# Performance work log

Hardware: AMD Instinct MI355X
Metric: run time of the kernel (lower is better)

Reference implementation:

```python
import jax, jax.numpy as jnp
import numpy as np

B, T = 32, 1000
NN, NB, CTX = 512, 16, 64
EMB = 256
DCAT = 3 * EMB
H, L = 256, 4
PN, PB = 512, 2
S, V = 8, 64


def setup_inputs() -> dict:
    key = jax.random.key(0)
    ks = jax.random.split(key, 20)
    r = lambda i, shape, sc=1.0: jax.random.normal(ks[i], shape, dtype=jnp.float32) * sc
    nu_log = jnp.log(-jnp.log(jax.random.uniform(ks[8], (L, H), minval=0.5, maxval=0.95)))
    inp = {
        'neural_input': r(0, (B, T, NN)),
        'behavior_input': r(1, (B, T, NB)),
        'session_id': jax.random.randint(ks[2], (B,), 0, V),
        'subject_id': jax.random.randint(ks[3], (B,), 0, S),
        'session_table': r(4, (V, CTX), 0.02),
        'neural_W': r(5, (S, EMB, NN), 1.0 / np.sqrt(NN)),
        'neural_b': jnp.zeros((S, EMB), jnp.float32),
        'behavior_W': r(6, (S, EMB, NB), 1.0 / np.sqrt(NB)),
        'behavior_b': jnp.zeros((S, EMB), jnp.float32),
        'ctx_W': r(7, (EMB, CTX), 1.0 / np.sqrt(CTX)),
        'ctx_b': jnp.zeros((EMB,), jnp.float32),
        'nu_log': nu_log,
        'theta_log': jnp.log(jax.random.uniform(ks[9], (L, H), minval=1e-4, maxval=6.283)),
        'gamma_log': 0.5 * jnp.log1p(-jnp.exp(-2.0 * jnp.exp(nu_log))),
        'B_re': r(10, (L, H, DCAT), 1.0 / np.sqrt(2 * DCAT)),
        'B_im': r(11, (L, H, DCAT), 1.0 / np.sqrt(2 * DCAT)),
        'C_re': r(12, (L, DCAT, H), 1.0 / np.sqrt(H)),
        'C_im': r(13, (L, DCAT, H), 1.0 / np.sqrt(H)),
        'D_skip': r(14, (L, DCAT)),
        'dec_n_W': r(15, (S, PN, DCAT), 1.0 / np.sqrt(DCAT)),
        'dec_n_b': jnp.zeros((S, PN), jnp.float32),
        'dec_b_W': r(16, (S, PB, DCAT), 1.0 / np.sqrt(DCAT)),
        'dec_b_b': jnp.zeros((S, PB), jnp.float32),
    }
    return inp


def _lru(u, nu_log, theta_log, gamma_log, B_re, B_im, C_re, C_im, D_skip):
    # Linear Recurrent Unit: complex diagonal recurrence x_t = lam*x_{t-1} + gamma*B u_t
    lam = jnp.exp(-jnp.exp(nu_log) + 1j * jnp.exp(theta_log))  # [H]
    g = jnp.exp(gamma_log)[:, None]
    Bu = (jnp.einsum('bti,hi->bth', u, B_re * g)
          + 1j * jnp.einsum('bti,hi->bth', u, B_im * g))  # [B,T,H] complex

    def step(x, bu_t):
        x = lam * x + bu_t
        return x, x

    x0 = jnp.zeros((u.shape[0], nu_log.shape[0]), jnp.complex64)
    _, xs = jax.lax.scan(step, x0, jnp.swapaxes(Bu, 0, 1))
    xs = jnp.swapaxes(xs, 0, 1)  # [B,T,H]
    y = jnp.einsum('bth,oh->bto', xs, C_re + 1j * C_im).real + D_skip * u
    return y


def _forward(neural_input, behavior_input, session_table, neural_W, neural_b,
             behavior_W, behavior_b, ctx_W, ctx_b, nu_log, theta_log, gamma_log,
             B_re, B_im, C_re, C_im, D_skip, dec_n_W, dec_n_b, dec_b_W, dec_b_b,
             session_id, subject_id):
    act = jax.nn.relu
    Bsz, Ts, _ = neural_input.shape
    # session-token embedding -> context embedder (Linear is per-timestep, so embed once then broadcast)
    ctx = act(session_table[session_id] @ ctx_W.T + ctx_b)  # [B,EMB]
    ctx = jnp.broadcast_to(ctx[:, None, :], (Bsz, Ts, ctx.shape[-1]))
    # subject-routed embedders: gather per-sample weights, one batched GEMM
    en = act(jnp.einsum('btf,bef->bte', neural_input, neural_W[subject_id])
             + neural_b[subject_id][:, None, :])
    eb = act(jnp.einsum('btf,bef->bte', behavior_input, behavior_W[subject_id])
             + behavior_b[subject_id][:, None, :])
    h = jnp.concatenate([en, eb, ctx], axis=-1)  # [B,T,3*EMB]
    for l in range(nu_log.shape[0]):
        h = _lru(h, nu_log[l], theta_log[l], gamma_log[l],
                 B_re[l], B_im[l], C_re[l], C_im[l], D_skip[l])
    # subject-routed decoders
    pred_n = jax.nn.softplus(jnp.einsum('btd,bod->bto', h, dec_n_W[subject_id])
                             + dec_n_b[subject_id][:, None, :])
    pred_b = (jnp.einsum('btd,bod->bto', h, dec_b_W[subject_id])
              + dec_b_b[subject_id][:, None, :])
    return pred_n, pred_b


def reference(neural_input, behavior_input, session_id, subject_id, session_table,
              neural_W, neural_b, behavior_W, behavior_b, ctx_W, ctx_b,
              nu_log, theta_log, gamma_log, B_re, B_im, C_re, C_im, D_skip,
              dec_n_W, dec_n_b, dec_b_W, dec_b_b):
    return _forward(neural_input, behavior_input, session_table, neural_W, neural_b,
                    behavior_W, behavior_b, ctx_W, ctx_b, nu_log, theta_log, gamma_log,
                    B_re, B_im, C_re, C_im, D_skip, dec_n_W, dec_n_b, dec_b_W, dec_b_b,
                    session_id, subject_id)
```

## Files before the change

kernel.cpp:

```cpp
#include <hip/hip_runtime.h>

typedef __bf16 bf16;
typedef __bf16 bf16x8 __attribute__((ext_vector_type(8)));
typedef float f32x4 __attribute__((ext_vector_type(4)));

#define AS1 __attribute__((address_space(1)))
#define AS3 __attribute__((address_space(3)))

__device__ __forceinline__ void gll16(const void* g, void* l) {
    __builtin_amdgcn_global_load_lds((const AS1 void*)g, (AS3 void*)l, 16, 0, 0);
}

template<int EPI>
__device__ __forceinline__
void gemm_body(const bf16* __restrict__ Abase, long long aBstride, int lda,
               const bf16* __restrict__ Wbase, long long wSstride,
               const float* __restrict__ biasBase, int biasStride,
               void* __restrict__ Cbase, long long cBstride, int ldc,
               const float* __restrict__ dskip,
               const bf16* __restrict__ Ubase, long long uBstride,
               const int* __restrict__ subj,
               int M, int K, int nbn, char* smem)
{
    const int tid = threadIdx.x;
    const int lane = tid & 63;
    const int wid = tid >> 6;
    const int wm = wid >> 1, wn = wid & 1;
    const int l15 = lane & 15, lhi = lane >> 4;
    const int sw7 = l15 & 7;

    const int nwg = gridDim.x;
    const int bid = blockIdx.x;
    const int q = nwg >> 3, r = nwg & 7;
    const int xcd = bid & 7;
    const int sw = xcd * q + (xcd < r ? xcd : r) + (bid >> 3);
    const int m0 = (sw / nbn) * 256;
    const int n0 = (sw % nbn) * 128;

    const int b = blockIdx.z;
    const int s = subj ? subj[b] : 0;
    const bf16* A = Abase + (size_t)b * aBstride;
    const bf16* W = Wbase + (size_t)s * wSstride;
    const float* bias = biasBase ? biasBase + (size_t)s * biasStride : nullptr;
    const bf16* U = Ubase ? Ubase + (size_t)b * uBstride : nullptr;
    const size_t coff = (size_t)b * cBstride;
    const int Mc = M - 1;

    f32x4 acc[4][4];
    #pragma unroll
    for (int i = 0; i < 4; ++i)
        #pragma unroll
        for (int j = 0; j < 4; ++j)
            acc[i][j] = f32x4{0.f, 0.f, 0.f, 0.f};

    int rA[4], rB[4];
    #pragma unroll
    for (int f = 0; f < 4; ++f) {
        rA[f] = (wm*64 + f*16 + l15) * 128;
        rB[f] = (wn*64 + f*16 + l15) * 128;
    }

    const int sub  = tid >> 3;
    const int slot = tid & 7;
    const int ldsw = (wid << 10);

    auto stage = [&](int kt, int bufo) {
        #pragma unroll
        for (int c = 0; c < 4; ++c) {
            const int row = c*64 + sub;
            const int gk = (kt << 6) + ((slot ^ (row & 7)) << 3);
            int ar = m0 + row; if (ar > Mc) ar = Mc;
            gll16(A + (size_t)ar * lda + gk, smem + bufo + c*8192 + ldsw);
        }
        #pragma unroll
        for (int c = 0; c < 2; ++c) {
            const int row = c*64 + sub;
            const int gk = (kt << 6) + ((slot ^ (row & 7)) << 3);
            gll16(W + (size_t)(n0 + row) * K + gk, smem + bufo + 32768 + c*8192 + ldsw);
        }
    };

    const int nkt = K >> 6;
    stage(0, 0);
    if (nkt > 1) stage(1, 49152);
    asm volatile("s_waitcnt vmcnt(6)" ::: "memory");
    __builtin_amdgcn_s_barrier();

    int curo = 0, nno = 98304;
    for (int t = 0; t < nkt; ++t) {
        if (t + 2 < nkt) stage(t + 2, nno);

        const char* cb = smem + curo;
        #pragma unroll
        for (int kk = 0; kk < 2; ++kk) {
            const int so_ = (((kk << 2) | lhi) ^ sw7) << 4;
            bf16x8 af[4], bg[4];
            #pragma unroll
            for (int f = 0; f < 4; ++f) af[f] = *(const bf16x8*)(cb + rA[f] + so_);
            #pragma unroll
            for (int g = 0; g < 4; ++g) bg[g] = *(const bf16x8*)(cb + 32768 + rB[g] + so_);
            #pragma unroll
            for (int i = 0; i < 4; ++i)
                #pragma unroll
                for (int j = 0; j < 4; ++j)
                    acc[i][j] = __builtin_amdgcn_mfma_f32_16x16x32_bf16(
                        af[i], bg[j], acc[i][j], 0, 0, 0);
        }

        if (t + 2 < nkt) {
            asm volatile("s_waitcnt vmcnt(6)" ::: "memory");
        } else if (t + 1 < nkt) {
            asm volatile("s_waitcnt vmcnt(0)" ::: "memory");
        }
        if (t + 1 < nkt) __builtin_amdgcn_s_barrier();

        curo = (curo == 98304) ? 0 : curo + 49152;
        nno  = (nno  == 98304) ? 0 : nno  + 49152;
    }

    __syncthreads();
    #pragma unroll
    for (int i = 0; i < 4; ++i) {
        #pragma unroll
        for (int j = 0; j < 4; ++j) {
            const int colb = (wn*64 + j*16 + l15) * 2;
            const f32x4 v = acc[i][j];
            #pragma unroll
            for (int qq = 0; qq < 4; ++qq) {
                const int row = wm*64 + i*16 + lhi*4 + qq;
                const int ad = row*256 + (colb & 15) + ((((colb >> 4) ^ (row & 7)) & 15) << 4);
                *(bf16*)(smem + ad) = (bf16)v[qq];
            }
        }
    }
    __syncthreads();

    #pragma unroll
    for (int u = 0; u < 8; ++u) {
        const int chunk = u*512 + tid;
        const int rr = chunk >> 4, ss = chunk & 15;
        const int gr = m0 + rr;
        if (gr >= M) continue;
        const int col = n0 + ss*8;
        const bf16x8 v = *(const bf16x8*)(smem + rr*256 + ((ss ^ (rr & 7)) << 4));
        if constexpr (EPI == 0) {
            const size_t ci = coff + (size_t)gr * ldc + col;
            *(bf16x8*)((bf16*)Cbase + ci) = v;
        } else if constexpr (EPI == 1) {
            const float4 b0 = *(const float4*)(bias + col);
            const float4 b1 = *(const float4*)(bias + col + 4);
            bf16x8 o;
            o[0] = (bf16)fmaxf((float)v[0] + b0.x, 0.f);
            o[1] = (bf16)fmaxf((float)v[1] + b0.y, 0.f);
            o[2] = (bf16)fmaxf((float)v[2] + b0.z, 0.f);
            o[3] = (bf16)fmaxf((float)v[3] + b0.w, 0.f);
            o[4] = (bf16)fmaxf((float)v[4] + b1.x, 0.f);
            o[5] = (bf16)fmaxf((float)v[5] + b1.y, 0.f);
            o[6] = (bf16)fmaxf((float)v[6] + b1.z, 0.f);
            o[7] = (bf16)fmaxf((float)v[7] + b1.w, 0.f);
            const size_t ci = coff + (size_t)gr * ldc + col;
            *(bf16x8*)((bf16*)Cbase + ci) = o;
        } else if constexpr (EPI == 2) {
            const bf16x8 uv = *(const bf16x8*)(U + (size_t)gr * ldc + col);
            const float4 d0 = *(const float4*)(dskip + col);
            const float4 d1 = *(const float4*)(dskip + col + 4);
            bf16x8 o;
            o[0] = (bf16)((float)v[0] + d0.x * (float)uv[0]);
            o[1] = (bf16)((float)v[1] + d0.y * (float)uv[1]);
            o[2] = (bf16)((float)v[2] + d0.z * (float)uv[2]);
            o[3] = (bf16)((float)v[3] + d0.w * (float)uv[3]);
            o[4] = (bf16)((float)v[4] + d1.x * (float)uv[4]);
            o[5] = (bf16)((float)v[5] + d1.y * (float)uv[5]);
            o[6] = (bf16)((float)v[6] + d1.z * (float)uv[6]);
            o[7] = (bf16)((float)v[7] + d1.w * (float)uv[7]);
            const size_t ci = coff + (size_t)gr * ldc + col;
            *(bf16x8*)((bf16*)Cbase + ci) = o;
        } else {
            const float4 b0 = *(const float4*)(bias + col);
            const float4 b1 = *(const float4*)(bias + col + 4);
            float xv[8];
            xv[0] = (float)v[0] + b0.x; xv[1] = (float)v[1] + b0.y;
            xv[2] = (float)v[2] + b0.z; xv[3] = (float)v[3] + b0.w;
            xv[4] = (float)v[4] + b1.x; xv[5] = (float)v[5] + b1.y;
            xv[6] = (float)v[6] + b1.z; xv[7] = (float)v[7] + b1.w;
            float4 o0, o1;
            #pragma unroll
            for (int e = 0; e < 8; ++e) {
                const float x = xv[e];
                const float sp = fmaxf(x, 0.f) + log1pf(expf(-fabsf(x)));
                if (e < 4) ((float*)&o0)[e] = sp; else ((float*)&o1)[e-4] = sp;
            }
            const size_t ci = coff + (size_t)gr * ldc + col;
            *(float4*)((float*)Cbase + ci) = o0;
            *(float4*)((float*)Cbase + ci + 4) = o1;
        }
    }
}

#define GEMM_WRAP(NAME, EPI)                                                     \
__global__ __launch_bounds__(512, 2)                                             \
void NAME(const bf16* __restrict__ Abase, long long aBstride, int lda,           \
          const bf16* __restrict__ Wbase, long long wSstride,                    \
          const float* __restrict__ biasBase, int biasStride,                    \
          void* __restrict__ Cbase, long long cBstride, int ldc,                 \
          const float* __restrict__ dskip,                                       \
          const bf16* __restrict__ Ubase, long long uBstride,                    \
          const int* __restrict__ subj, int M, int K, int nbn)                   \
{                                                                                \
    __shared__ char smem[147456];                                                \
    gemm_body<EPI>(Abase, aBstride, lda, Wbase, wSstride, biasBase, biasStride,  \
                   Cbase, cBstride, ldc, dskip, Ubase, uBstride, subj,           \
                   M, K, nbn, smem);                                             \
}
GEMM_WRAP(gemm_en,  1)
GEMM_WRAP(gemm_bu,  0)
GEMM_WRAP(gemm_y,   2)
GEMM_WRAP(gemm_dec, 3)

__global__ void scan_finals(const bf16* __restrict__ Bu,
                            const float* __restrict__ nu_log,
                            const float* __restrict__ theta_log,
                            float2* __restrict__ finals)
{
    const int g = blockIdx.x * 256 + threadIdx.x;
    const int h = g & 255;
    const int c = (g >> 8) % 40;
    const int b = g / 10240;
    const float a  = expf(nu_log[h]);
    const float th = expf(theta_log[h]);
    const float mag = expf(-a);
    const float lre = mag * cosf(th), lim = mag * sinf(th);
    float xre = 0.f, xim = 0.f;
    const bf16* p = Bu + ((size_t)(b*1000 + c*25)) * 512 + h;
    for (int i = 0; i < 25; ++i) {
        const float bre = (float)p[0], bim = (float)p[256];
        const float nre = lre*xre - lim*xim + bre;
        const float nim = lre*xim + lim*xre + bim;
        xre = nre; xim = nim;
        p += 512;
    }
    finals[(b*40 + c)*256 + h] = make_float2(xre, xim);
}

__global__ void scan_carry(const float2* __restrict__ finals,
                           float2* __restrict__ carry,
                           const float* __restrict__ nu_log,
                           const float* __restrict__ theta_log)
{
    const int g = blockIdx.x * 256 + threadIdx.x;
    const int h = g & 255;
    const int b = g >> 8;
    const float a  = expf(nu_log[h]);
    const float th = expf(theta_log[h]);
    const float mag = expf(-25.f * a);
    const float ang = 25.f * th;
    const float cre = mag * cosf(ang), cim = mag * sinf(ang);
    float pre = 0.f, pim = 0.f;
    for (int c = 0; c < 40; ++c) {
        const int idx = (b*40 + c)*256 + h;
        carry[idx] = make_float2(pre, pim);
        const float2 f = finals[idx];
        const float nre = f.x + cre*pre - cim*pim;
        const float nim = f.y + cre*pim + cim*pre;
        pre = nre; pim = nim;
    }
}

__global__ void scan_emit(const bf16* __restrict__ Bu,
                          const float2* __restrict__ carry,
                          const float* __restrict__ nu_log,
                          const float* __restrict__ theta_log,
                          bf16* __restrict__ xs)
{
    const int g = blockIdx.x * 256 + threadIdx.x;
    const int h = g & 255;
    const int c = (g >> 8) % 40;
    const int b = g / 10240;
    const float a  = expf(nu_log[h]);
    const float th = expf(theta_log[h]);
    const float mag = expf(-a);
    const float lre = mag * cosf(th), lim = mag * sinf(th);
    const float2 cr = carry[(b*40 + c)*256 + h];
    float xre = cr.x, xim = cr.y;
    const bf16* p = Bu + ((size_t)(b*1000 + c*25)) * 512 + h;
    bf16* qp = xs + ((size_t)(b*1000 + c*25)) * 512 + h;
    for (int i = 0; i < 25; ++i) {
        const float bre = (float)p[0], bim = (float)p[256];
        const float nre = lre*xre - lim*xim + bre;
        const float nim = lre*xim + lim*xre + bim;
        xre = nre; xim = nim;
        qp[0] = (bf16)xre; qp[256] = (bf16)xim;
        p += 512; qp += 512;
    }
}

__global__ void cast8_kern(const float* __restrict__ src, bf16* __restrict__ dst, int n8)
{
    const int i = blockIdx.x * 256 + threadIdx.x;
    if (i >= n8) return;
    const float4* s = (const float4*)src + (size_t)i*2;
    const float4 v0 = s[0], v1 = s[1];
    bf16x8 o;
    o[0] = (bf16)v0.x; o[1] = (bf16)v0.y; o[2] = (bf16)v0.z; o[3] = (bf16)v0.w;
    o[4] = (bf16)v1.x; o[5] = (bf16)v1.y; o[6] = (bf16)v1.z; o[7] = (bf16)v1.w;
    *((bf16x8*)dst + i) = o;
}

__global__ void packWB_kern(const float* __restrict__ Bre, const float* __restrict__ Bim,
                            const float* __restrict__ glog, bf16* __restrict__ WB)
{
    const int idx = blockIdx.x * 256 + threadIdx.x;
    if (idx >= 4*512*768) return;
    const int l = idx / (512*768);
    const int r = idx - l*(512*768);
    const int n = r / 768;
    const int k = r - n*768;
    float v;
    if (n < 256) v = Bre[((size_t)(l*256 + n))*768 + k] * expf(glog[l*256 + n]);
    else         v = Bim[((size_t)(l*256 + (n-256)))*768 + k] * expf(glog[l*256 + (n-256)]);
    WB[idx] = (bf16)v;
}

__global__ void packWC_kern(const float* __restrict__ Cre, const float* __restrict__ Cim,
                            bf16* __restrict__ WC)
{
    const int idx = blockIdx.x * 256 + threadIdx.x;
    if (idx >= 4*768*512) return;
    const int l = idx / (768*512);
    const int r = idx - l*(768*512);
    const int o = r / 512;
    const int k = r - o*512;
    const float v = (k < 256) ? Cre[((size_t)(l*768 + o))*256 + k]
                              : -Cim[((size_t)(l*768 + o))*256 + (k - 256)];
    WC[idx] = (bf16)v;
}

__global__ void ctx_kern(const float* __restrict__ st, const int* __restrict__ sess,
                         const float* __restrict__ cW, const float* __restrict__ cb,
                         float* __restrict__ ctx)
{
    const int b = blockIdx.x;
    const int e = threadIdx.x;
    const int sid = sess[b];
    const float* r = st + (size_t)sid * 64;
    const float* w = cW + (size_t)e * 64;
    float acc = cb[e];
    #pragma unroll 8
    for (int i = 0; i < 64; ++i) acc += r[i] * w[i];
    ctx[b*256 + e] = fmaxf(acc, 0.f);
}

__global__ void ebctx_kern(const float* __restrict__ behav,
                           const float* __restrict__ bW,
                           const float* __restrict__ bB,
                           const int* __restrict__ subj,
                           const float* __restrict__ ctx,
                           bf16* __restrict__ h0)
{
    const int b  = blockIdx.x >> 3;
    const int tc = blockIdx.x & 7;
    const int e = threadIdx.x;
    const int s = subj[b];
    float wreg[16];
    const float* w = bW + ((size_t)(s*256) + e)*16;
    #pragma unroll
    for (int i = 0; i < 16; ++i) wreg[i] = w[i];
    const float bb_ = bB[s*256 + e];
    const bf16 cx = (bf16)ctx[b*256 + e];
    const int t0 = tc * 125;
    for (int t = t0; t < t0 + 125; ++t) {
        const int blk = b*1000 + t;
        const float* bi = behav + (size_t)blk * 16;
        float acc = bb_;
        #pragma unroll
        for (int i = 0; i < 16; ++i) acc += bi[i] * wreg[i];
        bf16* hp = h0 + (size_t)blk * 768;
        hp[256 + e] = (bf16)fmaxf(acc, 0.f);
        hp[512 + e] = cx;
    }
}

__global__ void predb_kern(const bf16* __restrict__ h, const float* __restrict__ W,
                           const float* __restrict__ bb, const int* __restrict__ subj,
                           float* __restrict__ out)
{
    const int lane = threadIdx.x & 63;
    const int wid  = threadIdx.x >> 6;
    const int row  = blockIdx.x * 4 + wid;
    const int b = row / 1000;
    const int s = subj[b];
    const bf16* hr = h + (size_t)row * 768;
    const float* w0 = W + (size_t)(s*2) * 768;
    const float* w1 = w0 + 768;
    float a0 = 0.f, a1 = 0.f;
    #pragma unroll
    for (int j = 0; j < 12; ++j) {
        const int idx = j*64 + lane;
        const float hv = (float)hr[idx];
        a0 += hv * w0[idx];
        a1 += hv * w1[idx];
    }
    #pragma unroll
    for (int m = 32; m >= 1; m >>= 1) {
        a0 += __shfl_xor(a0, m);
        a1 += __shfl_xor(a1, m);
    }
    if (lane == 0) {
        out[(size_t)row*2 + 0] = a0 + bb[s*2 + 0];
        out[(size_t)row*2 + 1] = a1 + bb[s*2 + 1];
    }
}

extern "C" void kernel_launch(void* const* d_in, const int* in_sizes, int n_in,
                              void* d_out, int out_size, void* d_ws, size_t ws_size,
                              hipStream_t stream)
{
    const float* neural_input   = (const float*)d_in[0];
    const float* behavior_input = (const float*)d_in[1];
    const int*   session_id     = (const int*)d_in[2];
    const int*   subject_id     = (const int*)d_in[3];
    const float* session_table  = (const float*)d_in[4];
    const float* neural_W  = (const float*)d_in[5];
    const float* neural_b  = (const float*)d_in[6];
    const float* behavior_W = (const float*)d_in[7];
    const float* behavior_b = (const float*)d_in[8];
    const float* ctx_W = (const float*)d_in[9];
    const float* ctx_b = (const float*)d_in[10];
    const float* nu_log    = (const float*)d_in[11];
    const float* theta_log = (const float*)d_in[12];
    const float* gamma_log = (const float*)d_in[13];
    const float* B_re = (const float*)d_in[14];
    const float* B_im = (const float*)d_in[15];
    const float* C_re = (const float*)d_in[16];
    const float* C_im = (const float*)d_in[17];
    const float* D_skip = (const float*)d_in[18];
    const float* dec_n_W = (const float*)d_in[19];
    const float* dec_n_b = (const float*)d_in[20];
    const float* dec_b_W = (const float*)d_in[21];
    const float* dec_b_b = (const float*)d_in[22];
    float* out = (float*)d_out;

    char* ws = (char*)d_ws;
    size_t off = 0;
    auto alloc = [&](size_t bytes) -> char* {
        char* p = ws + off;
        off += (bytes + 255) & ~(size_t)255;
        return p;
    };
    bf16*   Wn      = (bf16*)alloc((size_t)8*256*512*2);
    bf16*   Wd      = (bf16*)alloc((size_t)8*512*768*2);
    bf16*   WB      = (bf16*)alloc((size_t)4*512*768*2);
    bf16*   WC      = (bf16*)alloc((size_t)4*768*512*2);
    float*  ctxbuf  = (float*)alloc((size_t)32*256*4);
    bf16*   hA      = (bf16*)alloc((size_t)32*1000*768*2);
    bf16*   hB      = (bf16*)alloc((size_t)32*1000*768*2);
    bf16*   xs      = (bf16*)alloc((size_t)32*1000*512*2);
    float2* finals  = (float2*)alloc((size_t)32*40*256*8);
    float2* carry   = (float2*)alloc((size_t)32*40*256*8);
    bf16*   Bu      = (bf16*)alloc((size_t)32*1000*512*2);
    bf16*   nbf     = Bu;

    cast8_kern<<<dim3(512),   256, 0, stream>>>(neural_W, Wn, 131072);
    cast8_kern<<<dim3(1536),  256, 0, stream>>>(dec_n_W,  Wd, 393216);
    packWB_kern<<<dim3(6144), 256, 0, stream>>>(B_re, B_im, gamma_log, WB);
    packWC_kern<<<dim3(6144), 256, 0, stream>>>(C_re, C_im, WC);
    ctx_kern<<<dim3(32), 256, 0, stream>>>(session_table, session_id, ctx_W, ctx_b, ctxbuf);
    cast8_kern<<<dim3(8000), 256, 0, stream>>>(neural_input, nbf, 2048000);

    ebctx_kern<<<dim3(256), 256, 0, stream>>>(behavior_input, behavior_W, behavior_b,
                                              subject_id, ctxbuf, hA);
    gemm_en<<<dim3(8, 1, 32), 512, 0, stream>>>(
        nbf, 512000LL, 512, Wn, 131072LL, neural_b, 256,
        hA, 768000LL, 768, nullptr, nullptr, 0LL, subject_id, 1000, 512, 2);

    for (int l = 0; l < 4; ++l) {
        const bf16* hin  = (l & 1) ? hB : hA;
        bf16*       hout = (l & 1) ? hA : hB;
        gemm_bu<<<dim3(500, 1, 1), 512, 0, stream>>>(
            hin, 0LL, 768, WB + (size_t)l*393216, 0LL, nullptr, 0,
            Bu, 0LL, 512, nullptr, nullptr, 0LL, nullptr, 32000, 768, 4);
        scan_finals<<<dim3(1280), 256, 0, stream>>>(Bu, nu_log + l*256, theta_log + l*256, finals);
        scan_carry<<<dim3(32), 256, 0, stream>>>(finals, carry, nu_log + l*256, theta_log + l*256);
        scan_emit<<<dim3(1280), 256, 0, stream>>>(Bu, carry, nu_log + l*256, theta_log + l*256, xs);
        gemm_y<<<dim3(750, 1, 1), 512, 0, stream>>>(
            xs, 0LL, 512, WC + (size_t)l*393216, 0LL, nullptr, 0,
            hout, 0LL, 768, D_skip + l*768, hin, 0LL, nullptr, 32000, 512, 6);
    }

    gemm_dec<<<dim3(16, 1, 32), 512, 0, stream>>>(
        hA, 768000LL, 768, Wd, 393216LL, dec_n_b, 512,
        out, 512000LL, 512, nullptr, nullptr, 0LL, subject_id, 1000, 768, 4);
    predb_kern<<<dim3(8000), 256, 0, stream>>>(hA, dec_b_W, dec_b_b, subject_id,
                                               out + 16384000);
}
```

Baseline: 610.6 us.

## Fuse three-pass chunked LRU scan into one kernel with in-block carry propagation

Replaces the finals/carry/emit kernel trio with a single kernel in which each block owns 32 hidden channels of one batch row, splits time into 8 chunks of 125 steps, and propagates chunk carries through shared memory. This removes two launches per layer and the global round-trips for the finals and carry buffers. The cost is much less parallelism: 256 blocks instead of 1280, each thread running a serial 125-step chain twice, and 32-channel loads that are less coalesced. It also switches the decoder softplus to fast __logf/__expf intrinsics, trading some accuracy.

After: 616.9 us. About the same (+1.0%).

```diff
diff --git a/kernel.cpp b/kernel.cpp
--- a/kernel.cpp
+++ b/kernel.cpp
@@ -1,6 +1,7 @@
 #include <hip/hip_runtime.h>
 
 typedef __bf16 bf16;
+typedef __bf16 bf16x2 __attribute__((ext_vector_type(2)));
 typedef __bf16 bf16x8 __attribute__((ext_vector_type(8)));
 typedef float f32x4 __attribute__((ext_vector_type(4)));
 
@@ -187,7 +188,7 @@
             #pragma unroll
             for (int e = 0; e < 8; ++e) {
                 const float x = xv[e];
-                const float sp = fmaxf(x, 0.f) + log1pf(expf(-fabsf(x)));
+                const float sp = fmaxf(x, 0.f) + __logf(1.f + __expf(-fabsf(x)));
                 if (e < 4) ((float*)&o0)[e] = sp; else ((float*)&o1)[e-4] = sp;
             }
             const size_t ci = coff + (size_t)gr * ldc + col;
@@ -217,80 +218,69 @@
 GEMM_WRAP(gemm_y,   2)
 GEMM_WRAP(gemm_dec, 3)
 
-__global__ void scan_finals(const bf16* __restrict__ Bu,
-                            const float* __restrict__ nu_log,
-                            const float* __restrict__ theta_log,
-                            float2* __restrict__ finals)
-{
-    const int g = blockIdx.x * 256 + threadIdx.x;
-    const int h = g & 255;
-    const int c = (g >> 8) % 40;
-    const int b = g / 10240;
+__global__ __launch_bounds__(256)
+void scan_fused(const bf16* __restrict__ Bu,
+                const float* __restrict__ nu_log,
+                const float* __restrict__ theta_log,
+                bf16* __restrict__ xs)
+{
+    const int b  = blockIdx.x >> 3;
+    const int hg = blockIdx.x & 7;
+    const int hl = threadIdx.x & 31;
+    const int c  = threadIdx.x >> 5;
+    const int h  = hg*32 + hl;
+
     const float a  = expf(nu_log[h]);
     const float th = expf(theta_log[h]);
     const float mag = expf(-a);
     const float lre = mag * cosf(th), lim = mag * sinf(th);
-    float xre = 0.f, xim = 0.f;
-    const bf16* p = Bu + ((size_t)(b*1000 + c*25)) * 512 + h;
-    for (int i = 0; i < 25; ++i) {
-        const float bre = (float)p[0], bim = (float)p[256];
-        const float nre = lre*xre - lim*xim + bre;
-        const float nim = lre*xim + lim*xre + bim;
-        xre = nre; xim = nim;
-        p += 512;
-    }
-    finals[(b*40 + c)*256 + h] = make_float2(xre, xim);
-}
-
-__global__ void scan_carry(const float2* __restrict__ finals,
-                           float2* __restrict__ carry,
-                           const float* __restrict__ nu_log,
-                           const float* __restrict__ theta_log)
-{
-    const int g = blockIdx.x * 256 + threadIdx.x;
-    const int h = g & 255;
-    const int b = g >> 8;
-    const float a  = expf(nu_log[h]);
-    const float th = expf(theta_log[h]);
-    const float mag = expf(-25.f * a);
-    const float ang = 25.f * th;
-    const float cre = mag * cosf(ang), cim = mag * sinf(ang);
-    float pre = 0.f, pim = 0.f;
-    for (int c = 0; c < 40; ++c) {
-        const int idx = (b*40 + c)*256 + h;
-        carry[idx] = make_float2(pre, pim);
-        const float2 f = finals[idx];
-        const float nre = f.x + cre*pre - cim*pim;
-        const float nim = f.y + cre*pim + cim*pre;
-        pre = nre; pim = nim;
-    }
-}
-
-__global__ void scan_emit(const bf16* __restrict__ Bu,
-                          const float2* __restrict__ carry,
-                          const float* __restrict__ nu_log,
-                          const float* __restrict__ theta_log,
-                          bf16* __restrict__ xs)
-{
-    const int g = blockIdx.x * 256 + threadIdx.x;
-    const int h = g & 255;
-    const int c = (g >> 8) % 40;
-    const int b = g / 10240;
-    const float a  = expf(nu_log[h]);
-    const float th = expf(theta_log[h]);
-    const float mag = expf(-a);
-    const float lre = mag * cosf(th), lim = mag * sinf(th);
-    const float2 cr = carry[(b*40 + c)*256 + h];
-    float xre = cr.x, xim = cr.y;
-    const bf16* p = Bu + ((size_t)(b*1000 + c*25)) * 512 + h;
-    bf16* qp = xs + ((size_t)(b*1000 + c*25)) * 512 + h;
-    for (int i = 0; i < 25; ++i) {
-        const float bre = (float)p[0], bim = (float)p[256];
-        const float nre = lre*xre - lim*xim + bre;
-        const float nim = lre*xim + lim*xre + bim;
-        xre = nre; xim = nim;
-        qp[0] = (bf16)xre; qp[256] = (bf16)xim;
-        p += 512; qp += 512;
+
+    const size_t base = ((size_t)(b*1000 + c*125)) * 512 + h;
+
+    {
+        const bf16* p = Bu + base;
+        float xre = 0.f, xim = 0.f;
+        for (int i = 0; i < 125; ++i) {
+            const float bre = (float)p[0], bim = (float)p[256];
+            const float nre = lre*xre - lim*xim + bre;
+            const float nim = lre*xim + lim*xre + bim;
+            xre = nre; xim = nim;
+            p += 512;
+        }
+        __shared__ float2 fin[8][32];
+        __shared__ float2 car[8][32];
+        fin[c][hl] = make_float2(xre, xim);
+        __syncthreads();
+
+        if (threadIdx.x < 32) {
+            const float m125 = expf(-125.f * a);
+            const float a125 = 125.f * th;
+            const float cre = m125 * cosf(a125), cim = m125 * sinf(a125);
+            float pre = 0.f, pim = 0.f;
+            #pragma unroll
+            for (int cc = 0; cc < 8; ++cc) {
+                car[cc][hl] = make_float2(pre, pim);
+                const float2 f = fin[cc][hl];
+                const float nre = f.x + cre*pre - cim*pim;
+                const float nim = f.y + cre*pim + cim*pre;
+                pre = nre; pim = nim;
+            }
+        }
+        __syncthreads();
+
+        const float2 cr = car[c][hl];
+        float yre = cr.x, yim = cr.y;
+        const bf16* pp = Bu + base;
+        bf16* qq = xs + base;
+        for (int i = 0; i < 125; ++i) {
+            const float bre = (float)pp[0], bim = (float)pp[256];
+            const float nre = lre*yre - lim*yim + bre;
+            const float nim = lre*yim + lim*yre + bim;
+            yre = nre; yim = nim;
+            qq[0]   = (bf16)yre;
+            qq[256] = (bf16)yim;
+            pp += 512; qq += 512;
+        }
     }
 }
 
@@ -455,8 +445,6 @@
     bf16*   hA      = (bf16*)alloc((size_t)32*1000*768*2);
     bf16*   hB      = (bf16*)alloc((size_t)32*1000*768*2);
     bf16*   xs      = (bf16*)alloc((size_t)32*1000*512*2);
-    float2* finals  = (float2*)alloc((size_t)32*40*256*8);
-    float2* carry   = (float2*)alloc((size_t)32*40*256*8);
     bf16*   Bu      = (bf16*)alloc((size_t)32*1000*512*2);
     bf16*   nbf     = Bu;
 
@@ -479,9 +467,7 @@
         gemm_bu<<<dim3(500, 1, 1), 512, 0, stream>>>(
             hin, 0LL, 768, WB + (size_t)l*393216, 0LL, nullptr, 0,
             Bu, 0LL, 512, nullptr, nullptr, 0LL, nullptr, 32000, 768, 4);
-        scan_finals<<<dim3(1280), 256, 0, stream>>>(Bu, nu_log + l*256, theta_log + l*256, finals);
-        scan_carry<<<dim3(32), 256, 0, stream>>>(finals, carry, nu_log + l*256, theta_log + l*256);
-        scan_emit<<<dim3(1280), 256, 0, stream>>>(Bu, carry, nu_log + l*256, theta_log + l*256, xs);
+        scan_fused<<<dim3(256), 256, 0, stream>>>(Bu, nu_log + l*256, theta_log + l*256, xs);
         gemm_y<<<dim3(750, 1, 1), 512, 0, stream>>>(
             xs, 0LL, 512, WC + (size_t)l*393216, 0LL, nullptr, 0,
             hout, 0LL, 768, D_skip + l*768, hin, 0LL, nullptr, 32000, 512, 6);
```
